# Kernel tuning notes

Measured on AMD Instinct MI355X. Metric: run time of the kernel, lower is better.

Reference implementation:

```python
import jax, jax.numpy as jnp
import numpy as np

B, NG, DEG, CW, OUT = 8, 16384, 16, 64, 256  # graphs, nodes/graph, avg degree, conv_width, output_dim


def _sage(x, src, dst, mask, Wl, bl, Wr):
    # PyG SAGEConv: mean-aggregate neighbors (src -> dst), lin_l(agg)+bias + lin_r(x)
    N = x.shape[0]
    s = jax.ops.segment_sum(x[src] * mask[:, None], dst, num_segments=N)
    c = jax.ops.segment_sum(mask, dst, num_segments=N)
    mean = s / jnp.maximum(c, 1.0)[:, None]
    return mean @ Wl.T + bl + x @ Wr.T


def _gcn(x, src, dst, mask, W, b):
    # PyG GCNConv: self-loops + symmetric deg^{-1/2} normalization; edge_weight == mask
    N = x.shape[0]
    xw = x @ W.T
    deg = 1.0 + jax.ops.segment_sum(mask, dst, num_segments=N)
    dis = jax.lax.rsqrt(deg)
    norm = dis[src] * mask * dis[dst]
    out = jax.ops.segment_sum(xw[src] * norm[:, None], dst, num_segments=N)
    return out + xw * (dis * dis)[:, None] + b


def _topk(x, src, dst, mask, w, n):
    # PyG TopKPooling: score = tanh(x.w/||w||), keep top ceil(0.5*n) per graph,
    # gate kept features by score, re-index edges (here: fixed-size edges + mask)
    score = jnp.tanh((x @ w) / jnp.linalg.norm(w))
    k = (n + 1) // 2
    vals, idx = jax.lax.top_k(score.reshape(B, n), k)  # [B,k], descending like PyG
    perm = (idx + (jnp.arange(B) * n)[:, None]).reshape(-1)  # global old indices
    x_new = x[perm] * vals.reshape(-1)[:, None]
    newpos = jnp.full((B * n,), -1, jnp.int32).at[perm].set(
        jnp.arange(B * k, dtype=jnp.int32))
    ns, nd = newpos[src], newpos[dst]
    m = mask * ((ns >= 0) & (nd >= 0)).astype(x.dtype)
    return x_new, jnp.maximum(ns, 0), jnp.maximum(nd, 0), m, k


def _readout(x, k):
    # [global_max_pool, global_mean_pool] per graph
    xr = x.reshape(B, k, -1)
    return jnp.concatenate([xr.max(axis=1), xr.mean(axis=1)], axis=1)


def setup_inputs() -> dict:
    key = jax.random.key(0)
    ks = jax.random.split(key, 24)
    N, Eg = B * NG, NG * DEG
    off = (jnp.arange(B) * NG)[:, None]
    src = (jax.random.randint(ks[0], (B, Eg), 0, NG) + off).reshape(-1)
    dst = (jax.random.randint(ks[1], (B, Eg), 0, NG) + off).reshape(-1)
    edge_index = jnp.stack([src, dst]).astype(jnp.int32)
    x = jax.random.normal(ks[2], (N, 2), jnp.float32)

    def xav(k, o, i):
        return jax.random.normal(k, (o, i), jnp.float32) * np.float32(np.sqrt(2.0 / (o + i)))

    def vec(k, d):
        return jax.random.normal(k, (d,), jnp.float32) * np.float32(1.0 / np.sqrt(d))

    return dict(
        x=x, edge_index=edge_index,
        Wl1=xav(ks[3], CW, 2), bl1=vec(ks[4], CW), Wr1=xav(ks[5], CW, 2),
        Wl2=xav(ks[6], CW, CW), bl2=vec(ks[7], CW), Wr2=xav(ks[8], CW, CW),
        W4=xav(ks[9], CW, CW), b4=vec(ks[10], CW),
        W5=xav(ks[11], CW, CW), b5=vec(ks[12], CW),
        wp1=vec(ks[13], CW), wp2=vec(ks[14], CW), wp4=vec(ks[15], CW), wp5=vec(ks[16], CW),
        Wa=xav(ks[17], 128, 2 * CW), ba=vec(ks[18], 128),
        Wb=xav(ks[19], 64, 128), bb=vec(ks[20], 64),
        Wc=xav(ks[21], OUT, 64), bc=vec(ks[22], OUT),
    )


def reference(x, edge_index, Wl1, bl1, Wr1, Wl2, bl2, Wr2, W4, b4, W5, b5,
              wp1, wp2, wp4, wp5, Wa, ba, Wb, bb, Wc, bc):
    src, dst = edge_index[0], edge_index[1]
    mask = jnp.ones(src.shape[0], x.dtype)
    n = NG
    h = jax.nn.relu(_sage(x, src, dst, mask, Wl1, bl1, Wr1))
    h, src, dst, mask, n = _topk(h, src, dst, mask, wp1, n)
    x1 = _readout(h, n)
    h = jax.nn.relu(_sage(h, src, dst, mask, Wl2, bl2, Wr2))
    h, src, dst, mask, n = _topk(h, src, dst, mask, wp2, n)
    x2 = _readout(h, n)
    h = jax.nn.relu(_gcn(h, src, dst, mask, W4, b4))
    h, src, dst, mask, n = _topk(h, src, dst, mask, wp4, n)
    x4 = _readout(h, n)
    h = jax.nn.relu(_gcn(h, src, dst, mask, W5, b5))
    h, src, dst, mask, n = _topk(h, src, dst, mask, wp5, n)
    x5 = _readout(h, n)
    z = x1 + x2 + x4 + x5  # [B, 2*CW]
    z = jax.nn.relu(z @ Wa.T + ba)
    z = jax.nn.relu(z @ Wb.T + bb)
    z = z @ Wc.T + bc
    return jax.nn.softmax(z, axis=1)
```

## Files before the change

kernel.cpp:

```cpp
#include <hip/hip_runtime.h>
#include <math.h>

constexpr int Bq  = 8;
constexpr int NGq = 16384;
constexpr int Nq  = Bq * NGq;
constexpr int Eq  = Nq * 16;
constexpr int Eg  = Eq / 8;

__global__ void k_prep(const float* __restrict__ Wl2, const float* __restrict__ Wr2,
                       const float* __restrict__ W4, const float* __restrict__ W5,
                       const float* __restrict__ Wa, const float* __restrict__ Wb,
                       const float* __restrict__ Wc,
                       const float* __restrict__ w1, const float* __restrict__ w2,
                       const float* __restrict__ w4p, const float* __restrict__ w5p,
                       float* __restrict__ wT, float* __restrict__ wMT,
                       float* __restrict__ winv, int* __restrict__ bsum) {
    int t = threadIdx.x, b = blockIdx.x;
    if (b < 4) {
        const float* in = (b == 0) ? Wl2 : (b == 1) ? Wr2 : (b == 2) ? W4 : W5;
        float* out = wT + (size_t)b * 4096;
        for (int i = t; i < 4096; i += 256) {
            int r = i >> 6, c = i & 63;
            out[c * 64 + r] = in[r * 64 + c];
        }
    } else if (b == 4) {
        float* WaT = wMT;
        for (int i = t; i < 16384; i += 256) {
            int r = i >> 7, c = i & 127;
            WaT[c * 128 + r] = Wa[r * 128 + c];
        }
    } else if (b == 5) {
        float* WbT = wMT + 16384;
        for (int i = t; i < 8192; i += 256) {
            int r = i >> 7, c = i & 127;
            WbT[c * 64 + r] = Wb[r * 128 + c];
        }
    } else if (b == 6) {
        float* WcT = wMT + 16384 + 8192;
        for (int i = t; i < 16384; i += 256) {
            int r = i >> 6, c = i & 63;
            WcT[c * 256 + r] = Wc[r * 64 + c];
        }
    } else {
        int vsel = t >> 6, lane = t & 63;
        const float* wp = (vsel == 0) ? w1 : (vsel == 1) ? w2 : (vsel == 2) ? w4p : w5p;
        float v = wp[lane];
        float ww = v * v;
        for (int o = 32; o; o >>= 1) ww += __shfl_xor(ww, o);
        if (lane == 0) winv[vsel] = 1.0f / sqrtf(ww);
        for (int i = t; i < 512; i += 256) bsum[i] = 0;
    }
}

__global__ void k_bcnt(const int* __restrict__ dst, int* __restrict__ bcnt) {
    __shared__ int hist[512];
    int t = threadIdx.x;
    int blk = blockIdx.x;
    if (t < 512) hist[t] = 0;
    __syncthreads();
    int e0 = blk * 8192;
#pragma unroll
    for (int i = 0; i < 8; i++) {
        int e = e0 + i * 1024 + t;
        atomicAdd(&hist[dst[e] >> 8], 1);
    }
    __syncthreads();
    if (t < 512) { int h = hist[t]; if (h) atomicAdd(&bcnt[t], h); }
}

__global__ void k_scan_b2(int* __restrict__ bsum, int* __restrict__ bcur) {
    __shared__ int s[512];
    int t = threadIdx.x;
    int own = bsum[t];
    s[t] = own;
    __syncthreads();
    for (int d = 1; d < 512; d <<= 1) {
        int v = (t >= d) ? s[t - d] : 0;
        __syncthreads();
        if (t >= d) s[t] += v;
        __syncthreads();
    }
    int ex = s[t] - own;
    bsum[t] = ex;
    bcur[t] = ex;
}

__global__ void k_csr_a(const int* __restrict__ src, const int* __restrict__ dst,
                        int* __restrict__ bcur, unsigned* __restrict__ pairs) {
    __shared__ int hist[512];
    __shared__ int base[512];
    __shared__ int lcur[512];
    int t = threadIdx.x;
    int blk = blockIdx.x;
    int e0 = blk * 8192;
    int bk[8]; unsigned p[8];
#pragma unroll
    for (int i = 0; i < 8; i++) {
        int e = e0 + i * 1024 + t;
        int d = dst[e];
        bk[i] = d >> 8;
        p[i] = ((unsigned)(d & 255) << 24) | (unsigned)src[e];
    }
    if (t < 512) hist[t] = 0;
    __syncthreads();
#pragma unroll
    for (int i = 0; i < 8; i++) atomicAdd(&hist[bk[i]], 1);
    __syncthreads();
    if (t < 512) {
        int h = hist[t];
        base[t] = h ? atomicAdd(&bcur[t], h) : 0;
        lcur[t] = 0;
    }
    __syncthreads();
#pragma unroll
    for (int i = 0; i < 8; i++) {
        int b = bk[i];
        int r = atomicAdd(&lcur[b], 1);
        pairs[base[b] + r] = p[i];
    }
}

__global__ void k_csr_b(const int* __restrict__ bsum, const unsigned* __restrict__ pairs,
                        const float2* __restrict__ x2,
                        int* __restrict__ off, int* __restrict__ csrc,
                        float2* __restrict__ mean) {
    __shared__ int lcnt[256];
    __shared__ int lcur[256];
    __shared__ int wsum[4];
    int b = blockIdx.x, t = threadIdx.x;
    int beg = bsum[b];
    int end = (b < 511) ? bsum[b + 1] : Eq;
    lcnt[t] = 0;
    __syncthreads();
    for (int i = beg + t; i < end; i += 256)
        atomicAdd(&lcnt[pairs[i] >> 24], 1);
    __syncthreads();
    int v = lcnt[t];
    int lane = t & 63, wv = t >> 6;
    int val = v;
    for (int o = 1; o < 64; o <<= 1) {
        int u = __shfl_up(val, o);
        if (lane >= o) val += u;
    }
    if (lane == 63) wsum[wv] = val;
    __syncthreads();
    int add = 0;
    for (int q = 0; q < wv; q++) add += wsum[q];
    int gpos = beg + val + add - v;
    off[b * 256 + t] = gpos;
    lcur[t] = gpos;
    if (b == 511 && t == 255) off[Nq] = Eq;
    __syncthreads();
    for (int i = beg + t; i < end; i += 256) {
        unsigned p = pairs[i];
        int pos = atomicAdd(&lcur[p >> 24], 1);
        csrc[pos] = (int)(p & 0x00FFFFFFu);
    }
    __syncthreads();
    float s0 = 0.f, s1 = 0.f;
    for (int e = gpos; e < gpos + v; e++) {
        float2 xv = x2[csrc[e]];
        s0 += xv.x; s1 += xv.y;
    }
    float c = fmaxf((float)v, 1.0f);
    mean[b * 256 + t] = make_float2(s0 / c, s1 / c);
}

__global__ void k_sage1e(const float* __restrict__ x, const float2* __restrict__ mean,
                         const float* __restrict__ Wl, const float* __restrict__ bl,
                         const float* __restrict__ Wr, const float* __restrict__ wp,
                         const float* __restrict__ invn,
                         float* __restrict__ out, float* __restrict__ score) {
    int blk = blockIdx.x;
    int g = blk & 7, i = blk >> 3;
    int wv = threadIdx.x >> 6, j = threadIdx.x & 63;
    int n = g * NGq + i * 4 + wv;
    float2 xn = ((const float2*)x)[n];
    float2 m = mean[n];
    float2 wl = ((const float2*)Wl)[j];
    float2 wr = ((const float2*)Wr)[j];
    float v = wl.x * m.x + wl.y * m.y + bl[j] + wr.x * xn.x + wr.y * xn.y;
    v = fmaxf(v, 0.f);
    out[n * 64 + j] = v;
    float d = v * wp[j];
    for (int o = 32; o; o >>= 1) d += __shfl_xor(d, o);
    if (j == 0) score[n] = d * invn[0];
}

template<int NM>
__global__ __launch_bounds__(256, 2)
void k_linf(const float* __restrict__ h, const int* __restrict__ perm,
            const float* __restrict__ score,
            const float* __restrict__ WaT, const float* __restrict__ WbT,
            const float* __restrict__ bias,
            float* __restrict__ oa, float* __restrict__ ob, int Nn, int linB,
            const int* __restrict__ off, const int* __restrict__ csrc,
            const int* __restrict__ map, const int* __restrict__ orig,
            float* __restrict__ dis, int ng, int disB,
            float* __restrict__ part, int kk, int G) {
    __shared__ float smx[256], ssm[256];
    int blk = blockIdx.x;
    if (blk < linB) {
        int j = threadIdx.x & 63, wv = threadIdx.x >> 6;
        float wa[64];
        float wb[NM == 2 ? 64 : 1];
#pragma unroll
        for (int q = 0; q < 64; q++) wa[q] = WaT[q * 64 + j];
        if constexpr (NM == 2) {
#pragma unroll
            for (int q = 0; q < 64; q++) wb[q] = WbT[q * 64 + j];
        }
        float bj = 0.f;
        if constexpr (NM == 2) bj = bias[j];
        int stride = linB * 4;
        for (int n = blk * 4 + wv; n < Nn; n += stride) {
            int p = perm[n];
            float sc = score[p];
            float iv = h[(size_t)p * 64 + j] * sc;
            float acca = 0.f;
            float accb = bj;
#pragma unroll
            for (int q = 0; q < 64; q++) {
                float s = __int_as_float(__builtin_amdgcn_readlane(__float_as_int(iv), q));
                acca += s * wa[q];
                if constexpr (NM == 2) accb += s * wb[q];
            }
            oa[(size_t)n * 64 + j] = acca;
            if constexpr (NM == 2) ob[(size_t)n * 64 + j] = accb;
        }
    } else if (blk < linB + disB) {
        int b2 = blk - linB;
        int g = b2 & 7, i = b2 >> 3;
        int wv = threadIdx.x >> 6, j = threadIdx.x & 63;
        int n = g * ng + i * 4 + wv;
        int o = orig[n];
        int beg = off[o], end = off[o + 1];
        int c = 0;
        for (int base = beg; base < end; base += 64) {
            int d = end - base; if (d > 64) d = 64;
            int cs = (j < d) ? map[csrc[base + j]] : -1;
            c += __popcll(__ballot(cs >= 0));
        }
        if (j == 0) dis[n] = 1.0f / sqrtf(1.0f + (float)c);
    } else {
        int b3 = blk - linB - disB;
        int b = b3 & 7, g = b3 >> 3;
        int rows = kk / G;
        int t = threadIdx.x, j = t & 63, q = t >> 6;
        const int* pb = perm + b * kk + g * rows;
        float mx = -3.0e38f, sm = 0.f;
        for (int i = q; i < rows; i += 4) {
            int row = pb[i];
            float v = h[(size_t)row * 64 + j] * score[row];
            mx = fmaxf(mx, v); sm += v;
        }
        smx[t] = mx; ssm[t] = sm;
        __syncthreads();
        if (q == 0) {
            for (int r = 1; r < 4; r++) { mx = fmaxf(mx, smx[j + 64 * r]); sm += ssm[j + 64 * r]; }
            part[(b * G + g) * 128 + j] = mx;
            part[(b * G + g) * 128 + 64 + j] = sm;
        }
    }
}

__global__ void k_readout_part(const float* __restrict__ h, const int* __restrict__ perm,
                               const float* __restrict__ score,
                               float* __restrict__ part, int k, int G) {
    __shared__ float smx[256], ssm[256];
    int blk = blockIdx.x;
    int b = blk & 7, g = blk >> 3;
    int rows = k / G;
    int t = threadIdx.x, j = t & 63, q = t >> 6;
    const int* pb = perm + b * k + g * rows;
    float mx = -3.0e38f, sm = 0.f;
    for (int i = q; i < rows; i += 4) {
        int row = pb[i];
        float v = h[(size_t)row * 64 + j] * score[row];
        mx = fmaxf(mx, v); sm += v;
    }
    smx[t] = mx; ssm[t] = sm;
    __syncthreads();
    if (q == 0) {
        for (int r = 1; r < 4; r++) { mx = fmaxf(mx, smx[j + 64 * r]); sm += ssm[j + 64 * r]; }
        part[(b * G + g) * 128 + j] = mx;
        part[(b * G + g) * 128 + 64 + j] = sm;
    }
}

__global__ void k_zfin(const float* __restrict__ part, float* __restrict__ z) {
    __shared__ float red[8][128];
    int b = blockIdx.x, t = threadIdx.x;
    int j = t & 127, s = t >> 7;
    const float* p; int g0;
    if (s < 4)       { p = part + (size_t)(b * 64) * 128;           g0 = s * 16; }
    else if (s < 6)  { p = part + 65536 + (size_t)(b * 32) * 128;   g0 = (s - 4) * 16; }
    else if (s == 6) { p = part + 98304 + (size_t)(b * 16) * 128;   g0 = 0; }
    else             { p = part + 114688 + (size_t)(b * 16) * 128;  g0 = 0; }
    float accm = -3.0e38f, accs = 0.f;
    for (int g = g0; g < g0 + 16; g++) {
        float v = p[g * 128 + j];
        accm = fmaxf(accm, v);
        accs += v;
    }
    red[s][j] = (j < 64) ? accm : accs;
    __syncthreads();
    if (s == 0) {
        float zv;
        if (j < 64) {
            float m1 = fmaxf(fmaxf(red[0][j], red[1][j]), fmaxf(red[2][j], red[3][j]));
            float m2 = fmaxf(red[4][j], red[5][j]);
            zv = m1 + m2 + red[6][j] + red[7][j];
        } else {
            float s1 = red[0][j] + red[1][j] + red[2][j] + red[3][j];
            float s2 = red[4][j] + red[5][j];
            zv = s1 / 8192.0f + s2 / 4096.0f + red[6][j] / 2048.0f + red[7][j] / 1024.0f;
        }
        z[b * 128 + j] = zv;
    }
}

template<int M>
__global__ void k_topk(float* __restrict__ score, int* __restrict__ newpos,
                       int* __restrict__ perm, int* __restrict__ map, int mode,
                       const int* __restrict__ orig_in, int* __restrict__ orig_out,
                       int og) {
    constexpr int n = M * 1024;
    constexpr int k = n / 2;
    __shared__ unsigned hist[256];
    __shared__ unsigned sh_pfx, sh_msk, sh_rem;
    __shared__ int sh_eqtot, sh_ctr;
    __shared__ int wtot[16];
    __shared__ int runTie, runGt;
    int t = threadIdx.x, b = blockIdx.x;
    int base = b * n;
    int lane = t & 63, wv = t >> 6;

    unsigned kr[M];
#pragma unroll
    for (int i = 0; i < M; i++) {
        unsigned u = __float_as_uint(score[base + t + (i << 10)]);
        kr[i] = u ^ ((u >> 31) ? 0xFFFFFFFFu : 0x80000000u);
    }
    if (t < 256) hist[t] = 0;
    if (t == 0) { sh_pfx = 0; sh_msk = 0; sh_rem = (unsigned)k;
                  sh_eqtot = 0; sh_ctr = 0; runTie = 0; runGt = 0; }
    __syncthreads();

    for (int shift = 24; shift >= 0; shift -= 8) {
        unsigned pfx = sh_pfx, msk = sh_msk;
#pragma unroll
        for (int i = 0; i < M; i++)
            if ((kr[i] & msk) == pfx) atomicAdd(&hist[(kr[i] >> shift) & 255], 1u);
        __syncthreads();
        if (t < 64) {
            unsigned rem = sh_rem;
            unsigned c0 = hist[255 - (t * 4 + 0)];
            unsigned c1 = hist[255 - (t * 4 + 1)];
            unsigned c2 = hist[255 - (t * 4 + 2)];
            unsigned c3 = hist[255 - (t * 4 + 3)];
            unsigned s = c0 + c1 + c2 + c3;
            unsigned sc = s;
            for (int o = 1; o < 64; o <<= 1) {
                unsigned u = __shfl_up(sc, o);
                if (t >= o) sc += u;
            }
            unsigned run = sc - s;
            unsigned cc[4] = {c0, c1, c2, c3};
#pragma unroll
            for (int q = 0; q < 4; q++) {
                unsigned incl = run + cc[q];
                if (run < rem && incl >= rem) {
                    int bb = 255 - (t * 4 + q);
                    sh_rem = rem - run;
                    sh_pfx = pfx | ((unsigned)bb << shift);
                    sh_msk = msk | (255u << shift);
                }
                run = incl;
            }
        }
        __syncthreads();
        if (t < 256) hist[t] = 0;
        __syncthreads();
    }
    unsigned K = sh_pfx;
    int T = (int)sh_rem;

    int le = 0;
#pragma unroll
    for (int i = 0; i < M; i++) le += (kr[i] == K) ? 1 : 0;
    for (int o = 32; o; o >>= 1) le += __shfl_xor(le, o);
    if (lane == 0) atomicAdd(&sh_eqtot, le);
    __syncthreads();

    if (sh_eqtot == T) {
#pragma unroll
        for (int i = 0; i < M; i++) {
            int cur = base + t + (i << 10);
            bool kept = kr[i] >= K;
            unsigned long long mk = __ballot(kept);
            int pos = 0;
            if (mk) {
                int fl = __ffsll(mk) - 1;
                int bp = 0;
                if (lane == fl) bp = atomicAdd(&sh_ctr, __popcll(mk));
                bp = __shfl(bp, fl);
                pos = bp + __popcll(mk & ((1ull << lane) - 1ull));
            }
            if (kept && pos < k) {
                newpos[cur] = b * k + pos;
                perm[b * k + pos] = cur;
                if (og) orig_out[b * k + pos] = (og == 1) ? cur : orig_in[cur];
                unsigned ob = (kr[i] & 0x80000000u) ? (kr[i] ^ 0x80000000u) : ~kr[i];
                score[cur] = tanhf(__uint_as_float(ob));
            } else newpos[cur] = -1;
        }
    } else {
        for (int i = 0; i < M; i++) {
            unsigned key = kr[i];
            int gt = key > K ? 1 : 0;
            int eq = key == K ? 1 : 0;
            int val = (eq << 16) | gt;
            for (int o = 1; o < 64; o <<= 1) {
                int v = __shfl_up(val, o);
                if (lane >= o) val += v;
            }
            if (lane == 63) wtot[wv] = val;
            __syncthreads();
            int add = 0;
            for (int q = 0; q < 16; q++) if (q < wv) add += wtot[q];
            val += add;
            int eqIncl = val >> 16, gtIncl = val & 0xffff;
            int eqExcl = eqIncl - eq, gtExcl = gtIncl - gt;
            int kept = gt | (eq & ((runTie + eqExcl) < T ? 1 : 0));
            int cur = base + t + (i << 10);
            if (kept) {
                int selEqBefore = runTie + eqExcl; if (selEqBefore > T) selEqBefore = T;
                int nl = runGt + gtExcl + selEqBefore;
                if (nl < k) {
                    newpos[cur] = b * k + nl;
                    perm[b * k + nl] = cur;
                    if (og) orig_out[b * k + nl] = (og == 1) ? cur : orig_in[cur];
                    unsigned ob = (key & 0x80000000u) ? (key ^ 0x80000000u) : ~key;
                    score[cur] = tanhf(__uint_as_float(ob));
                } else newpos[cur] = -1;
            } else newpos[cur] = -1;
            __syncthreads();
            if (t == 1023) { runTie += eqIncl; runGt += gtIncl; }
            __syncthreads();
        }
    }

    if (mode) {
        __syncthreads();
        int gbase = b * NGq;
        for (int i2 = t; i2 < NGq; i2 += 1024) {
            int gi = gbase + i2;
            if (mode == 1) map[gi] = newpos[gi];
            else { int m = map[gi]; map[gi] = (m >= 0) ? newpos[m] : -1; }
        }
    }
}

__global__ void k_sage_gather2(const float* __restrict__ gl, const int* __restrict__ off,
                               const int* __restrict__ csrc, const int* __restrict__ map,
                               const int* __restrict__ orig, const float* __restrict__ wp,
                               const float* __restrict__ invn,
                               float* __restrict__ out, float* __restrict__ score, int ng) {
    int blk = blockIdx.x;
    int g = blk & 7, i = blk >> 3;
    int wv = threadIdx.x >> 6, l = threadIdx.x & 63;
    int n = g * ng + i * 4 + wv;
    int o = orig[n];
    int beg = off[o], end = off[o + 1];
    int fg = l & 15, es = l >> 4;
    float4 own = make_float4(0.f, 0.f, 0.f, 0.f);
    if (es == 0) own = ((const float4*)(out + (size_t)n * 64))[fg];
    float4 acc = make_float4(0.f, 0.f, 0.f, 0.f);
    int cnt = 0;
    for (int base = beg; base < end; base += 64) {
        int d = end - base; if (d > 64) d = 64;
        int cs = (l < d) ? map[csrc[base + l]] : -1;
        cnt += __popcll(__ballot(cs >= 0));
        for (int e = 0; e < d; e += 4) {
            int c = __shfl(cs, e + es);
            if (c >= 0) {
                float4 v = ((const float4*)(gl + (size_t)c * 64))[fg];
                acc.x += v.x; acc.y += v.y; acc.z += v.z; acc.w += v.w;
            }
        }
    }
    acc.x += __shfl_xor(acc.x, 16); acc.y += __shfl_xor(acc.y, 16);
    acc.z += __shfl_xor(acc.z, 16); acc.w += __shfl_xor(acc.w, 16);
    acc.x += __shfl_xor(acc.x, 32); acc.y += __shfl_xor(acc.y, 32);
    acc.z += __shfl_xor(acc.z, 32); acc.w += __shfl_xor(acc.w, 32);
    float c = fmaxf((float)cnt, 1.0f);
    float4 v;
    v.x = fmaxf(acc.x / c + own.x, 0.f);
    v.y = fmaxf(acc.y / c + own.y, 0.f);
    v.z = fmaxf(acc.z / c + own.z, 0.f);
    v.w = fmaxf(acc.w / c + own.w, 0.f);
    float dsc = 0.f;
    if (es == 0) {
        ((float4*)(out + (size_t)n * 64))[fg] = v;
        float4 w4 = ((const float4*)wp)[fg];
        dsc = v.x * w4.x + v.y * w4.y + v.z * w4.z + v.w * w4.w;
    }
    for (int o2 = 32; o2; o2 >>= 1) dsc += __shfl_xor(dsc, o2);
    if (l == 0) score[n] = dsc * invn[0];
}

__global__ void k_gcn_gather(const float* __restrict__ xw, const int* __restrict__ off,
                             const int* __restrict__ csrc, const int* __restrict__ map,
                             const int* __restrict__ orig, const float* __restrict__ dis,
                             const float* __restrict__ bb, const float* __restrict__ wp,
                             const float* __restrict__ invn,
                             float* __restrict__ out, float* __restrict__ score, int ng) {
    int blk = blockIdx.x;
    int g = blk & 7, i = blk >> 3;
    int wv = threadIdx.x >> 6, l = threadIdx.x & 63;
    int n = g * ng + i * 4 + wv;
    int o = orig[n];
    int beg = off[o], end = off[o + 1];
    int fg = l & 15, es = l >> 4;
    float dn = dis[n];
    float4 own = make_float4(0.f, 0.f, 0.f, 0.f);
    if (es == 0) own = ((const float4*)(xw + (size_t)n * 64))[fg];
    float4 acc = make_float4(0.f, 0.f, 0.f, 0.f);
    for (int base = beg; base < end; base += 64) {
        int d = end - base; if (d > 64) d = 64;
        int cs = -1; float dsv = 0.f;
        if (l < d) {
            int cc = map[csrc[base + l]];
            if (cc >= 0) { cs = cc; dsv = dis[cc]; }
        }
        for (int e = 0; e < d; e += 4) {
            int c = __shfl(cs, e + es);
            float dv = __shfl(dsv, e + es);
            if (c >= 0) {
                float4 v = ((const float4*)(xw + (size_t)c * 64))[fg];
                acc.x += v.x * dv; acc.y += v.y * dv;
                acc.z += v.z * dv; acc.w += v.w * dv;
            }
        }
    }
    acc.x += __shfl_xor(acc.x, 16); acc.y += __shfl_xor(acc.y, 16);
    acc.z += __shfl_xor(acc.z, 16); acc.w += __shfl_xor(acc.w, 16);
    acc.x += __shfl_xor(acc.x, 32); acc.y += __shfl_xor(acc.y, 32);
    acc.z += __shfl_xor(acc.z, 32); acc.w += __shfl_xor(acc.w, 32);
    float dsc = 0.f;
    if (es == 0) {
        float4 b4 = ((const float4*)bb)[fg];
        float dd = dn * dn;
        float4 v;
        v.x = fmaxf(acc.x * dn + own.x * dd + b4.x, 0.f);
        v.y = fmaxf(acc.y * dn + own.y * dd + b4.y, 0.f);
        v.z = fmaxf(acc.z * dn + own.z * dd + b4.z, 0.f);
        v.w = fmaxf(acc.w * dn + own.w * dd + b4.w, 0.f);
        ((float4*)(out + (size_t)n * 64))[fg] = v;
        float4 w4 = ((const float4*)wp)[fg];
        dsc = v.x * w4.x + v.y * w4.y + v.z * w4.z + v.w * w4.w;
    }
    for (int o2 = 32; o2; o2 >>= 1) dsc += __shfl_xor(dsc, o2);
    if (l == 0) score[n] = dsc * invn[0];
}

__global__ void k_mlp(const float* __restrict__ z,
                      const float* __restrict__ WaT, const float* __restrict__ ba,
                      const float* __restrict__ WbT, const float* __restrict__ bb,
                      const float* __restrict__ WcT, const float* __restrict__ bc,
                      float* __restrict__ out) {
    __shared__ float sz[128];
    __shared__ float sa[128];
    __shared__ float sb2[64];
    __shared__ float sc[256];
    __shared__ float tmp[256];
    __shared__ float wred[4];
    int b = blockIdx.x, t = threadIdx.x;
    if (t < 128) sz[t] = z[b * 128 + t];
    __syncthreads();
    {
        int o = t & 127, half = t >> 7;
        float v = 0.f;
        int q0 = half * 64;
        for (int q = q0; q < q0 + 64; q++) v += sz[q] * WaT[q * 128 + o];
        tmp[t] = v;
        __syncthreads();
        if (t < 128) sa[t] = fmaxf(tmp[t] + tmp[t + 128] + ba[t], 0.f);
        __syncthreads();
    }
    {
        int o = t & 63, qr = t >> 6;
        float v = 0.f;
        int q0 = qr * 32;
        for (int q = q0; q < q0 + 32; q++) v += sa[q] * WbT[q * 64 + o];
        tmp[t] = v;
        __syncthreads();
        if (t < 64) sb2[t] = fmaxf(tmp[t] + tmp[t + 64] + tmp[t + 128] + tmp[t + 192] + bb[t], 0.f);
        __syncthreads();
    }
    {
        float v = bc[t];
        for (int q = 0; q < 64; q++) v += sb2[q] * WcT[q * 256 + t];
        sc[t] = v;
    }
    __syncthreads();
    float m = sc[t];
    for (int o2 = 32; o2; o2 >>= 1) m = fmaxf(m, __shfl_xor(m, o2));
    if ((t & 63) == 0) wred[t >> 6] = m;
    __syncthreads();
    m = fmaxf(fmaxf(wred[0], wred[1]), fmaxf(wred[2], wred[3]));
    __syncthreads();
    float e = expf(sc[t] - m);
    float s = e;
    for (int o2 = 32; o2; o2 >>= 1) s += __shfl_xor(s, o2);
    if ((t & 63) == 0) wred[t >> 6] = s;
    __syncthreads();
    s = wred[0] + wred[1] + wred[2] + wred[3];
    out[b * 256 + t] = e / s;
}

extern "C" void kernel_launch(void* const* d_in, const int* in_sizes, int n_in,
                              void* d_out, int out_size, void* d_ws, size_t ws_size,
                              hipStream_t stream) {
    const float* x   = (const float*)d_in[0];
    const int*   ei  = (const int*)d_in[1];
    const int* src = ei;
    const int* dst = ei + Eq;
    const float* Wl1 = (const float*)d_in[2];
    const float* bl1 = (const float*)d_in[3];
    const float* Wr1 = (const float*)d_in[4];
    const float* Wl2 = (const float*)d_in[5];
    const float* bl2 = (const float*)d_in[6];
    const float* Wr2 = (const float*)d_in[7];
    const float* W4  = (const float*)d_in[8];
    const float* b4  = (const float*)d_in[9];
    const float* W5  = (const float*)d_in[10];
    const float* b5  = (const float*)d_in[11];
    const float* wp1 = (const float*)d_in[12];
    const float* wp2 = (const float*)d_in[13];
    const float* wp4 = (const float*)d_in[14];
    const float* wp5 = (const float*)d_in[15];
    const float* Wa  = (const float*)d_in[16];
    const float* ba  = (const float*)d_in[17];
    const float* Wb  = (const float*)d_in[18];
    const float* bbv = (const float*)d_in[19];
    const float* Wc  = (const float*)d_in[20];
    const float* bc  = (const float*)d_in[21];
    float* out = (float*)d_out;

    const int N1 = Nq / 2, N2 = Nq / 4, N3 = Nq / 8, N4 = Nq / 16;

    char* w = (char*)d_ws;
    float* hA    = (float*)w; w += (size_t)Nq * 64 * 4;
    float* hB    = (float*)w; w += (size_t)N1 * 64 * 4;
    float* hC    = (float*)w; w += (size_t)N1 * 64 * 4;
    int*   csrc  = (int*)w;   w += (size_t)Eq * 4;
    int*   coff  = (int*)w;   w += (size_t)(Nq + 1) * 4;
    int*   bcur  = (int*)w;   w += (size_t)Nq * 4;
    int*   cnt   = (int*)w;   w += (size_t)Nq * 4;
    float* dis   = (float*)w; w += (size_t)Nq * 4;
    float* score = (float*)w; w += (size_t)Nq * 4;
    int*   newpos= (int*)w;   w += (size_t)Nq * 4;
    int*   map   = (int*)w;   w += (size_t)Nq * 4;
    int*   perm  = (int*)w;   w += (size_t)Nq * 4;
    int*   origA = (int*)w;   w += (size_t)Nq * 4;
    int*   origB = (int*)w;   w += (size_t)Nq * 4;
    int*   bsum  = (int*)w;   w += 512 * 4;
    float* part  = (float*)w; w += (size_t)131072 * 4;
    float* z     = (float*)w; w += 1024 * 4;
    float* wT    = (float*)w; w += 4 * 4096 * 4;
    float* wMT   = (float*)w; w += (16384 + 8192 + 16384) * 4;
    float* WlT2 = wT, *WrT2 = wT + 4096, *W4T = wT + 8192, *W5T = wT + 12288;
    float* WaT = wMT, *WbT = wMT + 16384, *WcT = wMT + 16384 + 8192;
    unsigned* pairs = (unsigned*)hA;
    float2* mean = (float2*)cnt;
    float* winv = (float*)(bcur + 1024);

    k_prep<<<8, 256, 0, stream>>>(Wl2, Wr2, W4, W5, Wa, Wb, Wc,
                                  wp1, wp2, wp4, wp5, wT, wMT, winv, bsum);
    k_bcnt<<<256, 1024, 0, stream>>>(dst, bsum);
    k_scan_b2<<<1, 512, 0, stream>>>(bsum, bcur);
    k_csr_a<<<256, 1024, 0, stream>>>(src, dst, bcur, pairs);
    k_csr_b<<<512, 256, 0, stream>>>(bsum, pairs, (const float2*)x, coff, csrc, mean);

    k_sage1e<<<Nq / 4, 256, 0, stream>>>(x, mean, Wl1, bl1, Wr1, wp1, winv, hA, score);
    k_topk<16><<<8, 1024, 0, stream>>>(score, newpos, perm, map, 1, nullptr, origA, 1);

    k_linf<2><<<1024 + 512, 256, 0, stream>>>(hA, perm, score, WlT2, WrT2, bl2,
                                              hC, hB, N1, 1024,
                                              nullptr, nullptr, nullptr, nullptr,
                                              nullptr, 0, 0,
                                              part, NGq / 2, 64);
    k_sage_gather2<<<N1 / 4, 256, 0, stream>>>(hC, coff, csrc, map, origA,
                                               wp2, winv + 1, hB, score, N1 / 8);
    k_topk<8><<<8, 1024, 0, stream>>>(score, newpos, perm, map, 2, origA, origB, 2);

    k_linf<1><<<512 + 8192 + 256, 256, 0, stream>>>(hB, perm, score, W4T, nullptr, nullptr,
                                                    hC, nullptr, N2, 512,
                                                    coff, csrc, map, origB, dis, N2 / 8, 8192,
                                                    part + 65536, NGq / 4, 32);
    k_gcn_gather<<<N2 / 4, 256, 0, stream>>>(hC, coff, csrc, map, origB, dis,
                                             b4, wp4, winv + 2, hB, score, N2 / 8);
    k_topk<4><<<8, 1024, 0, stream>>>(score, newpos, perm, map, 2, origB, origA, 2);

    k_linf<1><<<256 + 4096 + 128, 256, 0, stream>>>(hB, perm, score, W5T, nullptr, nullptr,
                                                    hC, nullptr, N3, 256,
                                                    coff, csrc, map, origA, dis, N3 / 8, 4096,
                                                    part + 98304, NGq / 8, 16);
    k_gcn_gather<<<N3 / 4, 256, 0, stream>>>(hC, coff, csrc, map, origA, dis,
                                             b5, wp5, winv + 3, hB, score, N3 / 8);
    k_topk<2><<<8, 1024, 0, stream>>>(score, newpos, perm, map, 0, nullptr, nullptr, 0);

    k_readout_part<<<8 * 16, 256, 0, stream>>>(hB, perm, score, part + 114688, NGq / 16, 16);
    k_zfin<<<8, 1024, 0, stream>>>(part, z);
    k_mlp<<<8, 256, 0, stream>>>(z, WaT, ba, WbT, bbv, WcT, bc, out);
}
```

Measured before the change: 452.7 us.

## Compact top-k rows into contiguous buffer before linear and readout stages

Adds a k_compact4 kernel after each top-k that gathers the kept rows, scales them by score, and writes them contiguously with float4 accesses. The linear, readout and gather kernels then read the compacted rows directly instead of indirecting through perm and score. The dual-matrix linear is split into two independent block ranges, each holding one 64-entry weight array with four partial accumulators, and launch bounds are raised to 4 blocks per CU for occupancy. The cost is four extra launches and an extra read and write of the kept features at each level.

```diff
diff --git a/kernel.cpp b/kernel.cpp
--- a/kernel.cpp
+++ b/kernel.cpp
@@ -187,49 +187,52 @@
     if (j == 0) score[n] = d * invn[0];
 }
 
-template<int NM>
-__global__ __launch_bounds__(256, 2)
-void k_linf(const float* __restrict__ h, const int* __restrict__ perm,
-            const float* __restrict__ score,
-            const float* __restrict__ WaT, const float* __restrict__ WbT,
-            const float* __restrict__ bias,
-            float* __restrict__ oa, float* __restrict__ ob, int Nn, int linB,
+__device__ __forceinline__
+void lin_rows(const float* __restrict__ h, const float* __restrict__ WT,
+              const float* __restrict__ bias, float* __restrict__ o,
+              int Nn, int nblk, int blk0) {
+    int j = threadIdx.x & 63, wv = threadIdx.x >> 6;
+    float wreg[64];
+#pragma unroll
+    for (int q = 0; q < 64; q++) wreg[q] = WT[q * 64 + j];
+    float bj = bias ? bias[j] : 0.f;
+    int stride = nblk * 4;
+    for (int n = blk0 * 4 + wv; n < Nn; n += stride) {
+        float iv = h[(size_t)n * 64 + j];
+        float a0 = 0.f, a1 = 0.f, a2 = 0.f, a3 = 0.f;
+#pragma unroll
+        for (int q = 0; q < 16; q++) {
+            float s0 = __int_as_float(__builtin_amdgcn_readlane(__float_as_int(iv), q));
+            float s1 = __int_as_float(__builtin_amdgcn_readlane(__float_as_int(iv), q + 16));
+            float s2 = __int_as_float(__builtin_amdgcn_readlane(__float_as_int(iv), q + 32));
+            float s3 = __int_as_float(__builtin_amdgcn_readlane(__float_as_int(iv), q + 48));
+            a0 += s0 * wreg[q];
+            a1 += s1 * wreg[q + 16];
+            a2 += s2 * wreg[q + 32];
+            a3 += s3 * wreg[q + 48];
+        }
+        o[(size_t)n * 64 + j] = (a0 + a1) + (a2 + a3) + bj;
+    }
+}
+
+__global__ __launch_bounds__(256, 4)
+void k_linf(const float* __restrict__ h,
+            const float* __restrict__ WT1, float* __restrict__ o1, int linB1,
+            const float* __restrict__ WT2, const float* __restrict__ bias,
+            float* __restrict__ o2, int linB2,
+            int Nn,
             const int* __restrict__ off, const int* __restrict__ csrc,
             const int* __restrict__ map, const int* __restrict__ orig,
             float* __restrict__ dis, int ng, int disB,
             float* __restrict__ part, int kk, int G) {
     __shared__ float smx[256], ssm[256];
     int blk = blockIdx.x;
-    if (blk < linB) {
-        int j = threadIdx.x & 63, wv = threadIdx.x >> 6;
-        float wa[64];
-        float wb[NM == 2 ? 64 : 1];
-#pragma unroll
-        for (int q = 0; q < 64; q++) wa[q] = WaT[q * 64 + j];
-        if constexpr (NM == 2) {
-#pragma unroll
-            for (int q = 0; q < 64; q++) wb[q] = WbT[q * 64 + j];
-        }
-        float bj = 0.f;
-        if constexpr (NM == 2) bj = bias[j];
-        int stride = linB * 4;
-        for (int n = blk * 4 + wv; n < Nn; n += stride) {
-            int p = perm[n];
-            float sc = score[p];
-            float iv = h[(size_t)p * 64 + j] * sc;
-            float acca = 0.f;
-            float accb = bj;
-#pragma unroll
-            for (int q = 0; q < 64; q++) {
-                float s = __int_as_float(__builtin_amdgcn_readlane(__float_as_int(iv), q));
-                acca += s * wa[q];
-                if constexpr (NM == 2) accb += s * wb[q];
-            }
-            oa[(size_t)n * 64 + j] = acca;
-            if constexpr (NM == 2) ob[(size_t)n * 64 + j] = accb;
-        }
-    } else if (blk < linB + disB) {
-        int b2 = blk - linB;
+    if (blk < linB1) {
+        lin_rows(h, WT1, nullptr, o1, Nn, linB1, blk);
+    } else if (blk < linB1 + linB2) {
+        lin_rows(h, WT2, bias, o2, Nn, linB2, blk - linB1);
+    } else if (blk < linB1 + linB2 + disB) {
+        int b2 = blk - linB1 - linB2;
         int g = b2 & 7, i = b2 >> 3;
         int wv = threadIdx.x >> 6, j = threadIdx.x & 63;
         int n = g * ng + i * 4 + wv;
@@ -243,15 +246,14 @@
         }
         if (j == 0) dis[n] = 1.0f / sqrtf(1.0f + (float)c);
     } else {
-        int b3 = blk - linB - disB;
+        int b3 = blk - linB1 - linB2 - disB;
         int b = b3 & 7, g = b3 >> 3;
         int rows = kk / G;
         int t = threadIdx.x, j = t & 63, q = t >> 6;
-        const int* pb = perm + b * kk + g * rows;
+        const float* basep = h + ((size_t)b * kk + (size_t)g * rows) * 64;
         float mx = -3.0e38f, sm = 0.f;
         for (int i = q; i < rows; i += 4) {
-            int row = pb[i];
-            float v = h[(size_t)row * 64 + j] * score[row];
+            float v = basep[i * 64 + j];
             mx = fmaxf(mx, v); sm += v;
         }
         smx[t] = mx; ssm[t] = sm;
@@ -264,19 +266,17 @@
     }
 }
 
-__global__ void k_readout_part(const float* __restrict__ h, const int* __restrict__ perm,
-                               const float* __restrict__ score,
-                               float* __restrict__ part, int k, int G) {
+__global__ void k_readout_part(const float* __restrict__ h, float* __restrict__ part,
+                               int k, int G) {
     __shared__ float smx[256], ssm[256];
     int blk = blockIdx.x;
     int b = blk & 7, g = blk >> 3;
     int rows = k / G;
     int t = threadIdx.x, j = t & 63, q = t >> 6;
-    const int* pb = perm + b * k + g * rows;
+    const float* basep = h + ((size_t)b * k + (size_t)g * rows) * 64;
     float mx = -3.0e38f, sm = 0.f;
     for (int i = q; i < rows; i += 4) {
-        int row = pb[i];
-        float v = h[(size_t)row * 64 + j] * score[row];
+        float v = basep[i * 64 + j];
         mx = fmaxf(mx, v); sm += v;
     }
     smx[t] = mx; ssm[t] = sm;
@@ -462,10 +462,25 @@
     }
 }
 
+__global__ void k_compact4(const float* __restrict__ hin, const float* __restrict__ score,
+                           const int* __restrict__ perm, float* __restrict__ hout, int k) {
+    int blk = blockIdx.x;
+    int g = blk & 7, i = blk >> 3;
+    int t = threadIdx.x;
+    int r = t >> 4, c = t & 15;
+    int nn = g * k + i * 16 + r;
+    int old = perm[nn];
+    float4 v = ((const float4*)(hin + (size_t)old * 64))[c];
+    float sc = score[old];
+    v.x *= sc; v.y *= sc; v.z *= sc; v.w *= sc;
+    ((float4*)(hout + (size_t)nn * 64))[c] = v;
+}
+
 __global__ void k_sage_gather2(const float* __restrict__ gl, const int* __restrict__ off,
                                const int* __restrict__ csrc, const int* __restrict__ map,
                                const int* __restrict__ orig, const float* __restrict__ wp,
                                const float* __restrict__ invn,
+                               float* __restrict__ own_in,
                                float* __restrict__ out, float* __restrict__ score, int ng) {
     int blk = blockIdx.x;
     int g = blk & 7, i = blk >> 3;
@@ -475,7 +490,7 @@
     int beg = off[o], end = off[o + 1];
     int fg = l & 15, es = l >> 4;
     float4 own = make_float4(0.f, 0.f, 0.f, 0.f);
-    if (es == 0) own = ((const float4*)(out + (size_t)n * 64))[fg];
+    if (es == 0) own = ((const float4*)(own_in + (size_t)n * 64))[fg];
     float4 acc = make_float4(0.f, 0.f, 0.f, 0.f);
     int cnt = 0;
     for (int base = beg; base < end; base += 64) {
@@ -686,33 +701,43 @@
 
     k_sage1e<<<Nq / 4, 256, 0, stream>>>(x, mean, Wl1, bl1, Wr1, wp1, winv, hA, score);
     k_topk<16><<<8, 1024, 0, stream>>>(score, newpos, perm, map, 1, nullptr, origA, 1);
-
-    k_linf<2><<<1024 + 512, 256, 0, stream>>>(hA, perm, score, WlT2, WrT2, bl2,
-                                              hC, hB, N1, 1024,
-                                              nullptr, nullptr, nullptr, nullptr,
-                                              nullptr, 0, 0,
-                                              part, NGq / 2, 64);
+    k_compact4<<<N1 / 16, 256, 0, stream>>>(hA, score, perm, hB, N1 / 8);
+
+    k_linf<<<512 + 512 + 512, 256, 0, stream>>>(hB,
+                                                WlT2, hC, 512,
+                                                WrT2, bl2, hA, 512,
+                                                N1,
+                                                nullptr, nullptr, nullptr, nullptr,
+                                                nullptr, 0, 0,
+                                                part, NGq / 2, 64);
     k_sage_gather2<<<N1 / 4, 256, 0, stream>>>(hC, coff, csrc, map, origA,
-                                               wp2, winv + 1, hB, score, N1 / 8);
+                                               wp2, winv + 1, hA, hA, score, N1 / 8);
     k_topk<8><<<8, 1024, 0, stream>>>(score, newpos, perm, map, 2, origA, origB, 2);
-
-    k_linf<1><<<512 + 8192 + 256, 256, 0, stream>>>(hB, perm, score, W4T, nullptr, nullptr,
-                                                    hC, nullptr, N2, 512,
-                                                    coff, csrc, map, origB, dis, N2 / 8, 8192,
-                                                    part + 65536, NGq / 4, 32);
+    k_compact4<<<N2 / 16, 256, 0, stream>>>(hA, score, perm, hB, N2 / 8);
+
+    k_linf<<<512 + 8192 + 256, 256, 0, stream>>>(hB,
+                                                 W4T, hC, 512,
+                                                 nullptr, nullptr, nullptr, 0,
+                                                 N2,
+                                                 coff, csrc, map, origB, dis, N2 / 8, 8192,
+                                                 part + 65536, NGq / 4, 32);
     k_gcn_gather<<<N2 / 4, 256, 0, stream>>>(hC, coff, csrc, map, origB, dis,
-                                             b4, wp4, winv + 2, hB, score, N2 / 8);
+                                             b4, wp4, winv + 2, hA, score, N2 / 8);
     k_topk<4><<<8, 1024, 0, stream>>>(score, newpos, perm, map, 2, origB, origA, 2);
-
-    k_linf<1><<<256 + 4096 + 128, 256, 0, stream>>>(hB, perm, score, W5T, nullptr, nullptr,
-                                                    hC, nullptr, N3, 256,
-                                                    coff, csrc, map, origA, dis, N3 / 8, 4096,
-                                                    part + 98304, NGq / 8, 16);
+    k_compact4<<<N3 / 16, 256, 0, stream>>>(hA, score, perm, hB, N3 / 8);
+
+    k_linf<<<256 + 4096 + 128, 256, 0, stream>>>(hB,
+                                                 W5T, hC, 256,
+                                                 nullptr, nullptr, nullptr, 0,
+                                                 N3,
+                                                 coff, csrc, map, origA, dis, N3 / 8, 4096,
+                                                 part + 98304, NGq / 8, 16);
     k_gcn_gather<<<N3 / 4, 256, 0, stream>>>(hC, coff, csrc, map, origA, dis,
-                                             b5, wp5, winv + 3, hB, score, N3 / 8);
+                                             b5, wp5, winv + 3, hA, score, N3 / 8);
     k_topk<2><<<8, 1024, 0, stream>>>(score, newpos, perm, map, 0, nullptr, nullptr, 0);
-
-    k_readout_part<<<8 * 16, 256, 0, stream>>>(hB, perm, score, part + 114688, NGq / 16, 16);
+    k_compact4<<<N4 / 16, 256, 0, stream>>>(hA, score, perm, hB, N4 / 8);
+
+    k_readout_part<<<8 * 16, 256, 0, stream>>>(hB, part + 114688, NGq / 16, 16);
     k_zfin<<<8, 1024, 0, stream>>>(part, z);
     k_mlp<<<8, 256, 0, stream>>>(z, WaT, ba, WbT, bbv, WcT, bc, out);
 }
```

New measurement: 439.5 us. -2.9%, faster.
